# Kernel tuning notes

Hardware: AMD Instinct MI355X
Metric: run time of the kernel (lower is better)

Reference implementation:

```python
import jax, jax.numpy as jnp
import numpy as np

D = 1024          # d_model
EXPAND = 2
DI = EXPAND * D   # d_inner = 2048
K = 4             # d_conv
B, L = 4, 2048
EPS = 1e-6


def setup_inputs() -> dict:
    key = jax.random.key(0)
    ks = jax.random.split(key, 16)
    n = lambda i, shape, scale=0.02: (jax.random.normal(ks[i], shape, jnp.float32) * scale)
    return {
        "x": jax.random.normal(ks[0], (B, L, D), jnp.float32),
        "norm_w": jnp.ones((D,), jnp.float32),
        "up_w": n(1, (D, DI)), "up_b": jnp.zeros((DI,), jnp.float32),
        "gate_w": n(2, (D, DI)), "gate_b": jnp.zeros((DI,), jnp.float32),
        "down_w": n(3, (DI, D)), "down_b": jnp.zeros((D,), jnp.float32),
        "conv_w": n(4, (DI, K), 0.2), "conv_b": jnp.zeros((DI,), jnp.float32),
        "wq": n(5, (D, D)), "wk": n(6, (D, D)), "wv": n(7, (D, D)), "wo": n(8, (D, D)),
        "decay": jnp.float32(0.99),
    }


def _rmsnorm(x, w):
    return x * jax.lax.rsqrt(jnp.mean(x * x, axis=-1, keepdims=True) + EPS) * w


def _forward(x, norm_w, up_w, up_b, gate_w, gate_b, down_w, down_b,
             conv_w, conv_b, wq, wk, wv, wo, decay):
    normed = _rmsnorm(x, norm_w)                              # [B,L,D]
    h = normed @ up_w + up_b                                  # [B,L,DI]
    # causal depthwise conv1d: left-pad K-1, groups = DI
    di = conv_w.shape[0]
    kern = conv_w.T[:, None, :]                               # [K,1,DI] (WIO)
    h = jax.lax.conv_general_dilated(
        h, kern, window_strides=(1,), padding=[(conv_w.shape[1] - 1, 0)],
        dimension_numbers=("NWC", "WIO", "NWC"), feature_group_count=di)
    h = jax.nn.silu(h + conv_b)                               # [B,L,DI]
    # gated MLP combine + down-projection
    out = (h * jax.nn.silu(normed @ gate_w + gate_b)) @ down_w + down_b  # [B,L,D]
    # Hebbian associative memory: M_t = decay*M_{t-1} + k_t^T v_t; y_t = q_t M_t
    q = out @ wq; k = out @ wk; v = out @ wv                  # [B,L,D]
    M0 = jnp.zeros((out.shape[0], out.shape[-1], out.shape[-1]), out.dtype)

    def step(M, qkv):
        qt, kt, vt = qkv                                      # each [B,D]
        M = decay * M + jnp.einsum("bd,be->bde", kt, vt)
        return M, jnp.einsum("bd,bde->be", qt, M)

    _, ys = jax.lax.scan(step, M0, (q.swapaxes(0, 1), k.swapaxes(0, 1), v.swapaxes(0, 1)))
    mem_out = ys.swapaxes(0, 1) @ wo                          # [B,L,D]
    return x + mem_out


def reference(x, norm_w, up_w, up_b, gate_w, gate_b, down_w, down_b,
              conv_w, conv_b, wq, wk, wv, wo, decay):
    return _forward(x, norm_w, up_w, up_b, gate_w, gate_b, down_w, down_b,
                    conv_w, conv_b, wq, wk, wv, wo, decay)
```

## Files before the change

### kernel.cpp

```cpp
#include <hip/hip_runtime.h>


typedef __bf16 bf16x8 __attribute__((ext_vector_type(8)));
typedef unsigned short u16x8 __attribute__((ext_vector_type(8)));
typedef float f32x4 __attribute__((ext_vector_type(4)));

constexpr int Bb = 4, Ll = 2048, Dd = 1024, DIc = 2048;
constexpr long LD  = (long)Ll * Dd;
constexpr long BLD = (long)Bb * LD;

static __device__ __forceinline__ unsigned short f2bf(float f) {
  unsigned u = __builtin_bit_cast(unsigned, f);
  u += 0x7fffu + ((u >> 16) & 1u);
  return (unsigned short)(u >> 16);
}
static __device__ __forceinline__ float bf2f(unsigned short u) {
  return __builtin_bit_cast(float, (unsigned)u << 16);
}
static __device__ __forceinline__ float silu(float g) {
  return g / (1.f + __expf(-g));
}

enum { EP_UG = 0, EP_DOWN, EP_GV, EP_DECAY, EP_YO };

#define STAGE_A(DBUF, MG, KH, TILE) {                                          \
    const int kt_ = ((TILE) < NTm1 ? (TILE) : NTm1);                           \
    __builtin_amdgcn_global_load_lds(                                          \
      (const __attribute__((address_space(1))) void*)                          \
        (Ag + (size_t)(aRow + (MG)*64) * lda + kt_*64 + (KH)*32 + aCol),       \
      (__attribute__((address_space(3))) void*)                                \
        (lds + (DBUF)*ADB + (KH)*AKH + (aRb + (MG)*4)*512), 16, 0, 0); }

#define STAGE_B(DBUF, NH, KH, TILE) {                                          \
    const int kt_ = ((TILE) < NTm1 ? (TILE) : NTm1);                           \
    __builtin_amdgcn_global_load_lds(                                          \
      (const __attribute__((address_space(1))) void*)                          \
        (Bg + (size_t)(bRow + (NH)*128) * ldb + kt_*64 + (KH)*32 + aCol),      \
      (__attribute__((address_space(3))) void*)                                \
        (lds + BOFF + (DBUF)*16384 + (KH)*8192 + ((NH)*8 + w)*512), 16, 0, 0); }

#define LOAD_A(DBUF, KS, MG) {                                                 \
  _Pragma("unroll") for (int j_ = 0; j_ < 4; ++j_)                             \
    af[j_] = *(const bf16x8*)&lds[(DBUF)*ADB + (KS)*AKH +                      \
        (aRdBase + (MG)*4 + j_)*512 + fr*32 + cph]; }

#define LOAD_B(DBUF, KS) {                                                     \
  _Pragma("unroll") for (int n_ = 0; n_ < 4; ++n_)                             \
    bfr[KS][n_] = *(const bf16x8*)&lds[BOFF + (DBUF)*16384 + (KS)*8192 +       \
        (bRb + n_)*512 + fr*32 + cph]; }

#define MFMA_PH(KS, MG) {                                                      \
  __builtin_amdgcn_s_setprio(1);                                               \
  _Pragma("unroll") for (int j_ = 0; j_ < 4; ++j_)                             \
  _Pragma("unroll") for (int n_ = 0; n_ < 4; ++n_)                             \
    acc[(MG)*4 + j_][n_] = __builtin_amdgcn_mfma_f32_16x16x32_bf16(            \
        af[j_], bfr[KS][n_], acc[(MG)*4 + j_][n_], 0, 0, 0);                   \
  __builtin_amdgcn_s_setprio(0); }

#define BAR() __builtin_amdgcn_s_barrier()
#define WAIT_LGKM0() { asm volatile("s_waitcnt lgkmcnt(0)" ::: "memory");      \
                       __builtin_amdgcn_sched_barrier(0); }
#define WAIT_LGKM8() asm volatile("s_waitcnt lgkmcnt(8)" ::: "memory")
#define WAIT_VM(N) asm volatile("s_waitcnt vmcnt(" #N ")" ::: "memory")

template <int EPI, int BM>
__global__ __launch_bounds__(512, 2) void gemm8_k(
    const ushort* __restrict__ A, const ushort* __restrict__ Bm,
    void* __restrict__ O0, const float* __restrict__ bias,
    const float* __restrict__ bias2, const float* __restrict__ xres,
    const float* __restrict__ decayp,
    int K, int lda, int ldb, int ldc,
    long sA, long sB, long sC,
    void* __restrict__ O1,
    const ushort* __restrict__ sA1, const ushort* __restrict__ sB1,
    ushort* __restrict__ sC1,
    const ushort* __restrict__ sA2, const ushort* __restrict__ sB2,
    ushort* __restrict__ sC2) {
  constexpr int MF = BM / 32;
  constexpr int ADB = BM * 64;
  constexpr int AKH = BM * 32;
  constexpr int BOFF = BM * 128;
  __shared__ ushort lds[BM == 256 ? 65536 : 49152];

  const int z = blockIdx.z;
  const int gx = gridDim.x;
  const int nwg = gx * gridDim.y;
  const int id = blockIdx.y * gx + blockIdx.x;
  const int chunk = nwg >> 3;
  const int swz = (id & 7) * chunk + (id >> 3);
  int m0 = (swz / gx) * BM;
  int n0 = (swz % gx) * 256;

  const int t = threadIdx.x;
  const int lane = t & 63;
  const int w = t >> 6;

  bool small = false;
  ushort* Cs = nullptr;
  const ushort* Ag;
  const ushort* Bg;
  if constexpr (EPI == EP_UG) {
    if (z == 1) {
      if (id >= 32) return;
      const int lid = id & 15;
      m0 = (lid >> 2) * 256;
      n0 = (lid & 3) * 256;
      if (id < 16) { Ag = sA1 + (size_t)m0 * 1024; Bg = sB1 + (size_t)n0 * 1024; Cs = sC1; }
      else         { Ag = sA2 + (size_t)m0 * 1024; Bg = sB2 + (size_t)n0 * 1024; Cs = sC2; }
      small = true;
    }
  }
  if constexpr (EPI == EP_DECAY) {
    if (n0 > m0) return;
  }
  if (!small) {
    Ag = A + (size_t)z * sA + (size_t)m0 * lda;
    Bg = Bm + (size_t)z * sB + (size_t)n0 * ldb;
  }

  int Kend = K;
  if constexpr (EPI == EP_YO) Kend = (K < m0 + BM) ? K : m0 + BM;
  const int NT = Kend >> 6;
  const int NTm1 = NT - 1;
  const int NI = NT >> 1;

  const int lp = lane ^ (((lane >> 5) & 1) << 1);
  const int aCol = (lp & 3) * 8;
  const int bRow = (w >> 2) * 64 + (w & 3) * 16 + (lp >> 2);
  int aRow, aRb, aRdBase;
  if constexpr (BM == 256) {
    aRow = (w >> 2) * 128 + (w & 3) * 16 + (lp >> 2);
    aRb = (w >> 2) * 8 + (w & 3);
    aRdBase = (w >> 2) * 8;
  } else {
    aRow = w * 16 + (lp >> 2);
    aRb = w;
    aRdBase = (w >> 2) * 4;
  }
  const int fr = lane & 15;
  const int kg = (lane >> 4) * 8;
  const int cph = kg ^ (((fr >> 3) & 1) << 4);
  const int bRb = ((w & 3) >> 1) * 8 + ((w & 3) & 1) * 4;

  f32x4 acc[MF][4] = {};
  bf16x8 af[4], bfr[2][4];

  if constexpr (BM == 256) {
    STAGE_A(0, 0, 0, 0); STAGE_A(0, 0, 1, 0); STAGE_A(0, 1, 0, 0); STAGE_A(0, 1, 1, 0);
    STAGE_B(0, 0, 0, 0); STAGE_B(0, 0, 1, 0); STAGE_B(0, 1, 0, 0); STAGE_B(0, 1, 1, 0);
    STAGE_B(1, 0, 0, 1); STAGE_B(1, 0, 1, 1); STAGE_B(1, 1, 0, 1); STAGE_B(1, 1, 1, 1);
    STAGE_A(1, 0, 0, 1); STAGE_A(1, 0, 1, 1);
    WAIT_VM(6);
    BAR();
    for (int i = 0; i < NI; ++i) {
      const int tt = 2 * i;
      LOAD_B(0, 0); LOAD_B(0, 1); LOAD_A(0, 0, 0);
      STAGE_A(1, 1, 0, tt + 1); STAGE_A(1, 1, 1, tt + 1);
      WAIT_LGKM8();
      BAR(); WAIT_LGKM0();
      MFMA_PH(0, 0);
      BAR();
      LOAD_A(0, 0, 1);
      STAGE_B(0, 0, 0, tt + 2); STAGE_B(0, 1, 0, tt + 2);
      BAR(); WAIT_LGKM0();
      MFMA_PH(0, 1);
      BAR();
      LOAD_A(0, 1, 0);
      STAGE_B(0, 0, 1, tt + 2); STAGE_B(0, 1, 1, tt + 2);
      BAR(); WAIT_LGKM0();
      MFMA_PH(1, 0);
      BAR();
      LOAD_A(0, 1, 1);
      STAGE_A(0, 0, 0, tt + 2); STAGE_A(0, 0, 1, tt + 2);
      WAIT_VM(6);
      BAR(); WAIT_LGKM0();
      MFMA_PH(1, 1);
      BAR();
      LOAD_B(1, 0); LOAD_B(1, 1); LOAD_A(1, 0, 0);
      STAGE_A(0, 1, 0, tt + 2); STAGE_A(0, 1, 1, tt + 2);
      WAIT_LGKM8();
      BAR(); WAIT_LGKM0();
      MFMA_PH(0, 0);
      BAR();
      LOAD_A(1, 0, 1);
      STAGE_B(1, 0, 0, tt + 3); STAGE_B(1, 1, 0, tt + 3);
      BAR(); WAIT_LGKM0();
      MFMA_PH(0, 1);
      BAR();
      LOAD_A(1, 1, 0);
      STAGE_B(1, 0, 1, tt + 3); STAGE_B(1, 1, 1, tt + 3);
      BAR(); WAIT_LGKM0();
      MFMA_PH(1, 0);
      BAR();
      LOAD_A(1, 1, 1);
      STAGE_A(1, 0, 0, tt + 3); STAGE_A(1, 0, 1, tt + 3);
      WAIT_VM(6);
      BAR(); WAIT_LGKM0();
      MFMA_PH(1, 1);
      BAR();
    }
  } else {
    STAGE_A(0, 0, 0, 0); STAGE_A(0, 0, 1, 0);
    STAGE_B(0, 0, 0, 0); STAGE_B(0, 1, 0, 0); STAGE_B(0, 0, 1, 0); STAGE_B(0, 1, 1, 0);
    STAGE_B(1, 0, 0, 1); STAGE_B(1, 1, 0, 1); STAGE_B(1, 0, 1, 1); STAGE_B(1, 1, 1, 1);
    WAIT_VM(4);
    BAR();
    for (int i = 0; i < NI; ++i) {
      const int tt = 2 * i;
      LOAD_B(0, 0); LOAD_B(0, 1); LOAD_A(0, 0, 0);
      STAGE_A(1, 0, 0, tt + 1); STAGE_A(1, 0, 1, tt + 1);
      WAIT_LGKM8();
      BAR(); WAIT_LGKM0();
      MFMA_PH(0, 0);
      BAR();
      LOAD_A(0, 1, 0);
      STAGE_B(0, 0, 0, tt + 2); STAGE_B(0, 1, 0, tt + 2);
      STAGE_B(0, 0, 1, tt + 2); STAGE_B(0, 1, 1, tt + 2);
      WAIT_VM(4);
      BAR(); WAIT_LGKM0();
      MFMA_PH(1, 0);
      BAR();
      LOAD_B(1, 0); LOAD_B(1, 1); LOAD_A(1, 0, 0);
      STAGE_A(0, 0, 0, tt + 2); STAGE_A(0, 0, 1, tt + 2);
      WAIT_LGKM8();
      BAR(); WAIT_LGKM0();
      MFMA_PH(0, 0);
      BAR();
      LOAD_A(1, 1, 0);
      STAGE_B(1, 0, 0, tt + 3); STAGE_B(1, 1, 0, tt + 3);
      STAGE_B(1, 0, 1, tt + 3); STAGE_B(1, 1, 1, tt + 3);
      WAIT_VM(4);
      BAR(); WAIT_LGKM0();
      MFMA_PH(1, 0);
      BAR();
    }
  }

  const int rb4 = (lane >> 4) * 4;
  const int wm = (w >> 2) * (BM / 2), wn = (w & 3) * 64;
  float logd = 0.f;
  if constexpr (EPI == EP_DECAY) logd = __logf(decayp[0]);

#pragma unroll
  for (int mf = 0; mf < MF; ++mf) {
#pragma unroll
    for (int nf = 0; nf < 4; ++nf) {
      const int gm0 = m0 + wm + mf * 16 + rb4;
      const int gn = n0 + wn + nf * 16 + fr;
      if constexpr (EPI == EP_GV) {
        if (gn < 1024) {
#pragma unroll
          for (int r = 0; r < 4; ++r)
            ((ushort*)O0)[(size_t)(gm0 + r) * 1024 + gn] = f2bf(acc[mf][nf][r]);
        } else {
          const int d = gn - 1024, b = gm0 >> 11, ttp = gm0 & 2047;
          ushort4 w4;
          w4.x = f2bf(acc[mf][nf][0]); w4.y = f2bf(acc[mf][nf][1]);
          w4.z = f2bf(acc[mf][nf][2]); w4.w = f2bf(acc[mf][nf][3]);
          *(ushort4*)&((ushort*)O1)[(size_t)b * LD + (size_t)d * Ll + ttp] = w4;
        }
      } else {
#pragma unroll
        for (int r = 0; r < 4; ++r) {
          const int gm = gm0 + r;
          const size_t idx = (size_t)z * sC + (size_t)gm * ldc + gn;
          const float v = acc[mf][nf][r];
          if constexpr (EPI == EP_UG) {
            if (small) {
              Cs[(size_t)gm * 1024 + gn] = f2bf(v);
            } else {
              const float b = (gn < 2048) ? bias[gn] : bias2[gn - 2048];
              ((ushort*)O0)[idx] = f2bf(v + b);
            }
          } else if constexpr (EPI == EP_DOWN) {
            ((ushort*)O0)[idx] = f2bf(v + bias[gn]);
          } else if constexpr (EPI == EP_DECAY) {
            ((ushort*)O0)[idx] =
                (gn <= gm) ? f2bf(v * __expf((float)(gm - gn) * logd)) : (ushort)0;
          } else {
            ((float*)O0)[idx] = v + xres[idx];
          }
        }
      }
    }
  }
}

__global__ __launch_bounds__(256) void prep_k(
    const float* __restrict__ up_w, const float* __restrict__ gate_w,
    const float* __restrict__ down_w, const float* __restrict__ wq,
    const float* __restrict__ wk, const float* __restrict__ wv,
    const float* __restrict__ wo, const float* __restrict__ conv_w,
    const float* __restrict__ x, const float* __restrict__ norm_w,
    ushort* __restrict__ ugw, ushort* __restrict__ down_wT,
    ushort* __restrict__ wq_bf, ushort* __restrict__ wk_bf,
    ushort* __restrict__ wv_bf, ushort* __restrict__ wo_T,
    ushort* __restrict__ cwT, ushort* __restrict__ nrm) {
  const int bid = blockIdx.x;
  const int t = threadIdx.x;
  if (bid < 7168) {
    const float* src; ushort* dst; int R, C, idx;
    if (bid < 2048)      { src = up_w;   dst = ugw;               R = 1024; C = 2048; idx = bid; }
    else if (bid < 4096) { src = gate_w; dst = ugw + 2048 * 1024; R = 1024; C = 2048; idx = bid - 2048; }
    else if (bid < 6144) { src = down_w; dst = down_wT;           R = 2048; C = 1024; idx = bid - 4096; }
    else                 { src = wo;     dst = wo_T;              R = 1024; C = 1024; idx = bid - 6144; }
    __shared__ float tile[32][33];
    const int tx = t & 31, ty = t >> 5;
    const int tilesx = C >> 5;
    const int c0 = (idx % tilesx) * 32, r0 = (idx / tilesx) * 32;
#pragma unroll
    for (int i = 0; i < 4; ++i)
      tile[ty + i * 8][tx] = src[(size_t)(r0 + ty + i * 8) * C + c0 + tx];
    __syncthreads();
#pragma unroll
    for (int i = 0; i < 4; ++i)
      dst[(size_t)(c0 + ty + i * 8) * R + r0 + tx] = f2bf(tile[tx][ty + i * 8]);
  } else if (bid < 10240) {
    const int seg = (bid - 7168) >> 10;
    const int idx = (bid - 7168) & 1023;
    const float* src = (seg == 0) ? wq : (seg == 1) ? wk : wv;
    ushort* dst = (seg == 0) ? wq_bf : (seg == 1) ? wk_bf : wv_bf;
    const size_t e = (size_t)idx * 1024 + t * 4;
    const float4 v = *(const float4*)(src + e);
    ushort4 r;
    r.x = f2bf(v.x); r.y = f2bf(v.y); r.z = f2bf(v.z); r.w = f2bf(v.w);
    *(ushort4*)(dst + e) = r;
  } else if (bid < 10248) {
    const int c = (bid - 10240) * 256 + t;
    const float4 v = *(const float4*)(conv_w + c * 4);
    cwT[0 * DIc + c] = f2bf(v.x);
    cwT[1 * DIc + c] = f2bf(v.y);
    cwT[2 * DIc + c] = f2bf(v.z);
    cwT[3 * DIc + c] = f2bf(v.w);
  } else {
    const int row = bid - 10248;
    const float* xr = x + (size_t)row * Dd;
    const float4 v = *(const float4*)(xr + t * 4);
    float ss = v.x * v.x + v.y * v.y + v.z * v.z + v.w * v.w;
#pragma unroll
    for (int m = 32; m; m >>= 1) ss += __shfl_xor(ss, m);
    __shared__ float red[4];
    if ((t & 63) == 0) red[t >> 6] = ss;
    __syncthreads();
    const float total = red[0] + red[1] + red[2] + red[3];
    const float rs = rsqrtf(total * (1.f / (float)Dd) + 1e-6f);
    const float4 wt = *(const float4*)(norm_w + t * 4);
    ushort4 r;
    r.x = f2bf(v.x * rs * wt.x); r.y = f2bf(v.y * rs * wt.y);
    r.z = f2bf(v.z * rs * wt.z); r.w = f2bf(v.w * rs * wt.w);
    *(ushort4*)(nrm + (size_t)row * Dd + t * 4) = r;
  }
}

__global__ __launch_bounds__(256) void conv_gate_k(
    const ushort* __restrict__ ug, const ushort* __restrict__ cwT,
    const float* __restrict__ cb, ushort* __restrict__ o) {
  const int t = threadIdx.x;
  const int cg = t & 31;
  const int ts = t >> 5;
  const int cblk = blockIdx.x & 7;
  const int rblk = blockIdx.x >> 3;
  const int c = cblk * 256 + cg * 8;
  const int row0 = rblk * 64 + ts * 8;

  u16x8 w[4];
#pragma unroll
  for (int k = 0; k < 4; ++k) w[k] = *(const u16x8*)&cwT[k * DIc + c];
  float wb[8];
  *(float4*)&wb[0] = *(const float4*)(cb + c);
  *(float4*)&wb[4] = *(const float4*)(cb + c + 4);

  u16x8 h3, h2, h1;
  if ((row0 & (Ll - 1)) == 0) {
    h3 = (u16x8){}; h2 = (u16x8){}; h1 = (u16x8){};
  } else {
    h3 = *(const u16x8*)&ug[(size_t)(row0 - 3) * 4096 + c];
    h2 = *(const u16x8*)&ug[(size_t)(row0 - 2) * 4096 + c];
    h1 = *(const u16x8*)&ug[(size_t)(row0 - 1) * 4096 + c];
  }

#pragma unroll
  for (int i = 0; i < 8; ++i) {
    const size_t rbase = (size_t)(row0 + i) * 4096;
    const u16x8 h0 = *(const u16x8*)&ug[rbase + c];
    const u16x8 g  = *(const u16x8*)&ug[rbase + 2048 + c];
    u16x8 ov;
#pragma unroll
    for (int j = 0; j < 8; ++j) {
      float acc = wb[j];
      acc += bf2f(w[0][j]) * bf2f(h3[j]);
      acc += bf2f(w[1][j]) * bf2f(h2[j]);
      acc += bf2f(w[2][j]) * bf2f(h1[j]);
      acc += bf2f(w[3][j]) * bf2f(h0[j]);
      ov[j] = f2bf(silu(acc) * silu(bf2f(g[j])));
    }
    *(u16x8*)&o[(size_t)(row0 + i) * DIc + c] = ov;
    h3 = h2; h2 = h1; h1 = h0;
  }
}

extern "C" void kernel_launch(void* const* d_in, const int* in_sizes, int n_in,
                              void* d_out, int out_size, void* d_ws,
                              size_t ws_size, hipStream_t stream) {
  const float* x      = (const float*)d_in[0];
  const float* norm_w = (const float*)d_in[1];
  const float* up_w   = (const float*)d_in[2];
  const float* up_b   = (const float*)d_in[3];
  const float* gate_w = (const float*)d_in[4];
  const float* gate_b = (const float*)d_in[5];
  const float* down_w = (const float*)d_in[6];
  const float* down_b = (const float*)d_in[7];
  const float* conv_w = (const float*)d_in[8];
  const float* conv_b = (const float*)d_in[9];
  const float* wq     = (const float*)d_in[10];
  const float* wk     = (const float*)d_in[11];
  const float* wv     = (const float*)d_in[12];
  const float* wo     = (const float*)d_in[13];
  const float* decay  = (const float*)d_in[14];
  float* out = (float*)d_out;
  char* w8 = (char*)d_ws;

  const size_t MiB = 1u << 20;
  ushort* nrm      = (ushort*)(w8 + 0 * MiB);
  ushort* ug       = (ushort*)(w8 + 16 * MiB);
  ushort* S        = (ushort*)(w8 + 16 * MiB);
  ushort* combined = (ushort*)(w8 + 80 * MiB);
  ushort* G        = (ushort*)(w8 + 112 * MiB);
  ushort* vT       = (ushort*)(w8 + 144 * MiB);
  ushort* ugw      = (ushort*)(w8 + 176 * MiB);
  ushort* down_wT  = (ushort*)(w8 + 184 * MiB);
  ushort* wq_bf    = (ushort*)(w8 + 188 * MiB);
  ushort* wk_bf    = (ushort*)(w8 + 190 * MiB);
  ushort* wv_bf    = (ushort*)(w8 + 192 * MiB);
  ushort* wo_T     = (ushort*)(w8 + 194 * MiB);
  ushort* WsT      = (ushort*)(w8 + 196 * MiB);
  ushort* Wv2T     = (ushort*)(w8 + 198 * MiB);
  ushort* cwT      = (ushort*)(w8 + 200 * MiB);

  prep_k<<<18440, 256, 0, stream>>>(up_w, gate_w, down_w, wq, wk, wv, wo,
                                    conv_w, x, norm_w,
                                    ugw, down_wT, wq_bf, wk_bf, wv_bf, wo_T,
                                    cwT, nrm);

  gemm8_k<EP_UG, 256><<<dim3(16, 32, 2), 512, 0, stream>>>(
      nrm, ugw, ug, up_b, gate_b, nullptr, nullptr,
      1024, 1024, 1024, 4096, 0, 0, 0, nullptr,
      wk_bf, wq_bf, WsT, wo_T, wv_bf, Wv2T);

  conv_gate_k<<<1024, 256, 0, stream>>>(ug, cwT, conv_b, combined);

  gemm8_k<EP_DOWN, 128><<<dim3(4, 64), 512, 0, stream>>>(
      combined, down_wT, nrm, down_b, nullptr, nullptr, nullptr,
      2048, 2048, 2048, 1024, 0, 0, 0, nullptr,
      nullptr, nullptr, nullptr, nullptr, nullptr, nullptr);

  gemm8_k<EP_GV, 128><<<dim3(8, 64), 512, 0, stream>>>(
      nrm, WsT, G, nullptr, nullptr, nullptr, nullptr,
      1024, 1024, 1024, 1024, 0, 0, 0, vT,
      nullptr, nullptr, nullptr, nullptr, nullptr, nullptr);

  gemm8_k<EP_DECAY, 256><<<dim3(8, 8, Bb), 512, 0, stream>>>(
      G, nrm, S, nullptr, nullptr, nullptr, decay,
      1024, 1024, 1024, 2048, LD, LD, (long)Ll * Ll, nullptr,
      nullptr, nullptr, nullptr, nullptr, nullptr, nullptr);

  gemm8_k<EP_YO, 128><<<dim3(4, 16, Bb), 512, 0, stream>>>(
      S, vT, out, nullptr, nullptr, x, nullptr,
      2048, 2048, 2048, 1024, (long)Ll * Ll, LD, LD, nullptr,
      nullptr, nullptr, nullptr, nullptr, nullptr, nullptr);
}
```

Before: 322.3 us.

## Move weight-product GEMMs from up/gate GEMM launch into conv_gate kernel

The two small 1024x1024 weight-product GEMMs (wk·wq and wo·wv), which were packed as a second z-slice of the large up/gate GEMM launch, are moved into 128 extra blocks of the conv_gate kernel. Those blocks use a simple 128x128 MFMA tile with direct global-to-LDS loads. This removes the z=1 branch overhead and the mostly-idle second grid slice from the big GEMM, letting that launch run as a uniform 256-thread-free grid. The cost is that the conv kernel's tail may be lengthened by the slower, non-pipelined small GEMM blocks.

```diff
diff --git a/kernel.cpp b/kernel.cpp
--- a/kernel.cpp
+++ b/kernel.cpp
@@ -71,11 +71,7 @@
     const float* __restrict__ decayp,
     int K, int lda, int ldb, int ldc,
     long sA, long sB, long sC,
-    void* __restrict__ O1,
-    const ushort* __restrict__ sA1, const ushort* __restrict__ sB1,
-    ushort* __restrict__ sC1,
-    const ushort* __restrict__ sA2, const ushort* __restrict__ sB2,
-    ushort* __restrict__ sC2) {
+    void* __restrict__ O1) {
   constexpr int MF = BM / 32;
   constexpr int ADB = BM * 64;
   constexpr int AKH = BM * 32;
@@ -88,35 +84,18 @@
   const int id = blockIdx.y * gx + blockIdx.x;
   const int chunk = nwg >> 3;
   const int swz = (id & 7) * chunk + (id >> 3);
-  int m0 = (swz / gx) * BM;
-  int n0 = (swz % gx) * 256;
+  const int m0 = (swz / gx) * BM;
+  const int n0 = (swz % gx) * 256;
 
   const int t = threadIdx.x;
   const int lane = t & 63;
   const int w = t >> 6;
 
-  bool small = false;
-  ushort* Cs = nullptr;
-  const ushort* Ag;
-  const ushort* Bg;
-  if constexpr (EPI == EP_UG) {
-    if (z == 1) {
-      if (id >= 32) return;
-      const int lid = id & 15;
-      m0 = (lid >> 2) * 256;
-      n0 = (lid & 3) * 256;
-      if (id < 16) { Ag = sA1 + (size_t)m0 * 1024; Bg = sB1 + (size_t)n0 * 1024; Cs = sC1; }
-      else         { Ag = sA2 + (size_t)m0 * 1024; Bg = sB2 + (size_t)n0 * 1024; Cs = sC2; }
-      small = true;
-    }
-  }
   if constexpr (EPI == EP_DECAY) {
     if (n0 > m0) return;
   }
-  if (!small) {
-    Ag = A + (size_t)z * sA + (size_t)m0 * lda;
-    Bg = Bm + (size_t)z * sB + (size_t)n0 * ldb;
-  }
+  const ushort* Ag = A + (size_t)z * sA + (size_t)m0 * lda;
+  const ushort* Bg = Bm + (size_t)z * sB + (size_t)n0 * ldb;
 
   int Kend = K;
   if constexpr (EPI == EP_YO) Kend = (K < m0 + BM) ? K : m0 + BM;
@@ -266,12 +245,8 @@
           const size_t idx = (size_t)z * sC + (size_t)gm * ldc + gn;
           const float v = acc[mf][nf][r];
           if constexpr (EPI == EP_UG) {
-            if (small) {
-              Cs[(size_t)gm * 1024 + gn] = f2bf(v);
-            } else {
-              const float b = (gn < 2048) ? bias[gn] : bias2[gn - 2048];
-              ((ushort*)O0)[idx] = f2bf(v + b);
-            }
+            const float b = (gn < 2048) ? bias[gn] : bias2[gn - 2048];
+            ((ushort*)O0)[idx] = f2bf(v + b);
           } else if constexpr (EPI == EP_DOWN) {
             ((ushort*)O0)[idx] = f2bf(v + bias[gn]);
           } else if constexpr (EPI == EP_DECAY) {
@@ -354,12 +329,72 @@
 
 __global__ __launch_bounds__(256) void conv_gate_k(
     const ushort* __restrict__ ug, const ushort* __restrict__ cwT,
-    const float* __restrict__ cb, ushort* __restrict__ o) {
+    const float* __restrict__ cb, ushort* __restrict__ o,
+    const ushort* __restrict__ wk_bf, const ushort* __restrict__ wq_bf,
+    const ushort* __restrict__ wo_T, const ushort* __restrict__ wv_bf,
+    ushort* __restrict__ WsT, ushort* __restrict__ Wv2T) {
+  const int bid = blockIdx.x;
   const int t = threadIdx.x;
+  if (bid < 128) {
+    __shared__ ushort lds[8192];
+    ushort* As = lds;
+    ushort* Bs = lds + 4096;
+    const int oo = bid >> 6, lid = bid & 63;
+    const int m0 = (lid >> 3) * 128, n0 = (lid & 7) * 128;
+    const ushort* A = (oo ? wo_T : wk_bf) + (size_t)m0 * 1024;
+    const ushort* B = (oo ? wv_bf : wq_bf) + (size_t)n0 * 1024;
+    ushort* C = oo ? Wv2T : WsT;
+    const int lane = t & 63, wave = t >> 6;
+    const int wm = (wave >> 1) * 64, wn = (wave & 1) * 64;
+    const int fr = lane & 15, kg = (lane >> 4) * 8;
+    const int srow0 = wave * 16 + (lane >> 2), scol = (lane & 3) * 8;
+    f32x4 acc[4][4] = {};
+    for (int k0 = 0; k0 < 1024; k0 += 32) {
+#pragma unroll
+      for (int p = 0; p < 2; ++p) {
+        __builtin_amdgcn_global_load_lds(
+            (const __attribute__((address_space(1))) void*)
+                (A + (size_t)(srow0 + p * 64) * 1024 + k0 + scol),
+            (__attribute__((address_space(3))) void*)(As + (p * 4 + wave) * 512),
+            16, 0, 0);
+        __builtin_amdgcn_global_load_lds(
+            (const __attribute__((address_space(1))) void*)
+                (B + (size_t)(srow0 + p * 64) * 1024 + k0 + scol),
+            (__attribute__((address_space(3))) void*)(Bs + (p * 4 + wave) * 512),
+            16, 0, 0);
+      }
+      __syncthreads();
+      bf16x8 af[4], bv[4];
+#pragma unroll
+      for (int i = 0; i < 4; ++i) {
+        af[i] = *(const bf16x8*)&As[(wm + i * 16 + fr) * 32 + kg];
+        bv[i] = *(const bf16x8*)&Bs[(wn + i * 16 + fr) * 32 + kg];
+      }
+#pragma unroll
+      for (int mi = 0; mi < 4; ++mi)
+#pragma unroll
+        for (int ni = 0; ni < 4; ++ni)
+          acc[mi][ni] = __builtin_amdgcn_mfma_f32_16x16x32_bf16(
+              af[mi], bv[ni], acc[mi][ni], 0, 0, 0);
+      __syncthreads();
+    }
+    const int rb = (lane >> 4) * 4;
+#pragma unroll
+    for (int mi = 0; mi < 4; ++mi)
+#pragma unroll
+      for (int ni = 0; ni < 4; ++ni)
+#pragma unroll
+        for (int r = 0; r < 4; ++r)
+          C[(size_t)(m0 + wm + mi * 16 + rb + r) * 1024 + n0 + wn + ni * 16 + fr] =
+              f2bf(acc[mi][ni][r]);
+    return;
+  }
+
+  const int cbid = bid - 128;
   const int cg = t & 31;
   const int ts = t >> 5;
-  const int cblk = blockIdx.x & 7;
-  const int rblk = blockIdx.x >> 3;
+  const int cblk = cbid & 7;
+  const int rblk = cbid >> 3;
   const int c = cblk * 256 + cg * 8;
   const int row0 = rblk * 64 + ts * 8;
 
@@ -442,30 +477,26 @@
                                     ugw, down_wT, wq_bf, wk_bf, wv_bf, wo_T,
                                     cwT, nrm);
 
-  gemm8_k<EP_UG, 256><<<dim3(16, 32, 2), 512, 0, stream>>>(
+  gemm8_k<EP_UG, 256><<<dim3(16, 32), 512, 0, stream>>>(
       nrm, ugw, ug, up_b, gate_b, nullptr, nullptr,
-      1024, 1024, 1024, 4096, 0, 0, 0, nullptr,
-      wk_bf, wq_bf, WsT, wo_T, wv_bf, Wv2T);
-
-  conv_gate_k<<<1024, 256, 0, stream>>>(ug, cwT, conv_b, combined);
+      1024, 1024, 1024, 4096, 0, 0, 0, nullptr);
+
+  conv_gate_k<<<1152, 256, 0, stream>>>(ug, cwT, conv_b, combined,
+                                        wk_bf, wq_bf, wo_T, wv_bf, WsT, Wv2T);
 
   gemm8_k<EP_DOWN, 128><<<dim3(4, 64), 512, 0, stream>>>(
       combined, down_wT, nrm, down_b, nullptr, nullptr, nullptr,
-      2048, 2048, 2048, 1024, 0, 0, 0, nullptr,
-      nullptr, nullptr, nullptr, nullptr, nullptr, nullptr);
+      2048, 2048, 2048, 1024, 0, 0, 0, nullptr);
 
   gemm8_k<EP_GV, 128><<<dim3(8, 64), 512, 0, stream>>>(
       nrm, WsT, G, nullptr, nullptr, nullptr, nullptr,
-      1024, 1024, 1024, 1024, 0, 0, 0, vT,
-      nullptr, nullptr, nullptr, nullptr, nullptr, nullptr);
+      1024, 1024, 1024, 1024, 0, 0, 0, vT);
 
   gemm8_k<EP_DECAY, 256><<<dim3(8, 8, Bb), 512, 0, stream>>>(
       G, nrm, S, nullptr, nullptr, nullptr, decay,
-      1024, 1024, 1024, 2048, LD, LD, (long)Ll * Ll, nullptr,
-      nullptr, nullptr, nullptr, nullptr, nullptr, nullptr);
+      1024, 1024, 1024, 2048, LD, LD, (long)Ll * Ll, nullptr);
 
   gemm8_k<EP_YO, 128><<<dim3(4, 16, Bb), 512, 0, stream>>>(
       S, vT, out, nullptr, nullptr, x, nullptr,
-      2048, 2048, 2048, 1024, (long)Ll * Ll, LD, LD, nullptr,
-      nullptr, nullptr, nullptr, nullptr, nullptr, nullptr);
-}
+      2048, 2048, 2048, 1024, (long)Ll * Ll, LD, LD, nullptr);
+}
```

Result: faster. 280.5 us (-13.0%).
